# Kernel tuning notes

Hardware: AMD Instinct MI355X
Metric: run time of the kernel (lower is better)

Reference implementation:

```python
import jax, jax.numpy as jnp
import numpy as np

B, T, D, C, L, H = 8192, 128, 1, 1, 1, 64


def _mlp(x, w1, b1, w2, b2):
    # Linear -> Softplus -> Linear
    return jax.nn.softplus(x @ w1 + b1) @ w2 + b2


def setup_inputs() -> dict:
    key = jax.random.key(0)
    ks = jax.random.split(key, 32)
    s = 0.1

    def w(k, shape):
        return jax.random.normal(k, shape, jnp.float32) * s

    p = {}
    p["xs"] = jax.random.normal(ks[0], (T, B, D), jnp.float32)
    p["ts"] = jnp.arange(T, dtype=jnp.float32)
    p["noise_std"] = jnp.float32(5.0)
    p["eps0"] = jax.random.normal(ks[1], (B, L), jnp.float32)
    p["dW_std"] = jax.random.normal(ks[2], (T - 1, B, L), jnp.float32)
    # encoder: data -> hidden -> context
    p["ew1"] = w(ks[3], (D, H)); p["eb1"] = w(ks[4], (H,))
    p["ew2"] = w(ks[5], (H, C)); p["eb2"] = w(ks[6], (C,))
    # qz0_net: context -> 2*latent
    p["qw"] = w(ks[7], (C, 2 * L)); p["qb"] = w(ks[8], (2 * L,))
    # f_net: latent+context -> hidden -> latent
    p["fw1"] = w(ks[9], (L + C, H)); p["fb1"] = w(ks[10], (H,))
    p["fw2"] = w(ks[11], (H, L)); p["fb2"] = w(ks[12], (L,))
    # h_net: latent -> hidden -> latent
    p["hw1"] = w(ks[13], (L, H)); p["hb1"] = w(ks[14], (H,))
    p["hw2"] = w(ks[15], (H, L)); p["hb2"] = w(ks[16], (L,))
    # g_nets: L independent 1 -> hidden -> 1 -> sigmoid nets, stacked on leading L axis
    p["gw1"] = w(ks[17], (L, H)); p["gb1"] = w(ks[18], (L, H))
    p["gw2"] = w(ks[19], (L, H)); p["gb2"] = w(ks[20], (L,))
    # projector: latent -> hidden -> data
    p["pw1"] = w(ks[21], (L, H)); p["pb1"] = w(ks[22], (H,))
    p["pw2"] = w(ks[23], (H, D)); p["pb2"] = w(ks[24], (D,))
    p["pz0_mean"] = jnp.zeros((1, L), jnp.float32)
    p["pz0_logstd"] = jnp.zeros((1, L), jnp.float32)
    return p


def reference(xs, ts, noise_std, eps0, dW_std,
              ew1, eb1, ew2, eb2, qw, qb,
              fw1, fb1, fw2, fb2, hw1, hb1, hw2, hb2,
              gw1, gb1, gw2, gb2, pw1, pb1, pw2, pb2,
              pz0_mean, pz0_logstd):
    Tn = ts.shape[0]
    # ctx = flip(encoder(flip(xs)))  (encoder is pointwise in time)
    ctx = jnp.flip(_mlp(jnp.flip(xs, axis=0), ew1, eb1, ew2, eb2), axis=0)  # [T,B,C]
    qz = ctx[0] @ qw + qb
    qm, qls = jnp.split(qz, 2, axis=1)  # [B,L] each
    z0 = qm + jnp.exp(qls) * eps0

    def g_fn(z):  # per-coordinate diagonal diffusion nets
        hid = jax.nn.softplus(z[:, :, None] * gw1[None] + gb1[None])  # [B,L,H]
        return jax.nn.sigmoid(jnp.einsum('blh,lh->bl', hid, gw2) + gb2)

    def step(z, inp):
        k, dwk = inp
        t = ts[k]
        dt = ts[k + 1] - ts[k]
        idx = jnp.minimum(jnp.searchsorted(ts, t, side='right'), Tn - 1)
        c = jnp.take(ctx, idx, axis=0)  # [B,C]
        fv = _mlp(jnp.concatenate([z, c], axis=1), fw1, fb1, fw2, fb2)
        hv = _mlp(z, hw1, hb1, hw2, hb2)
        gv = g_fn(z)
        u = (fv - hv) / gv
        lr = 0.5 * jnp.sum(u * u, axis=1) * dt  # logqp path increment [B]
        z_next = z + fv * dt + gv * dwk * jnp.sqrt(dt)  # Euler-Maruyama
        return z_next, (z_next, lr)

    _, (ztail, log_ratio) = jax.lax.scan(step, z0, (jnp.arange(Tn - 1), dW_std))
    zs = jnp.concatenate([z0[None], ztail], axis=0)  # [T,B,L]
    _xs = _mlp(zs, pw1, pb1, pw2, pb2)  # [T,B,D]
    lp = -0.5 * ((xs - _xs) / noise_std) ** 2 - jnp.log(noise_std) - 0.5 * jnp.log(2 * jnp.pi)
    log_pxs = lp.sum(axis=(0, 2)).mean()
    kl = (pz0_logstd - qls) + (jnp.exp(2 * qls) + (qm - pz0_mean) ** 2) / (2 * jnp.exp(2 * pz0_logstd)) - 0.5
    logqp0 = kl.sum(axis=1).mean()
    logqp_path = log_ratio.sum(axis=0).mean()
    return (log_pxs, logqp0 + logqp_path)
```

## Files before the change

### kernel.cpp

```cpp
#include <hip/hip_runtime.h>
#include <math.h>


#define B_SZ 8192
#define T_SZ 128
#define NBLK 16

#define FQ1_OFF  0
#define HGP1_OFF 8196
#define FQ2_OFF  12296
#define HGP2_OFF 16396
#define ET2_OFF  20496
#define TAB_FLOATS 22544
#define FQ1_I  0
#define HGP1_I 2049
#define FQ2_I  3074
#define HGP2_I 4099

#define NF1 2049
#define NH1 1025
#define NF2 1025
#define NH2 1025
#define NEE 1024
#define NENT (NF1+NH1+NF2+NH2+NEE)

#define NXI 1024
#define XSF 64.0f
#define XOF 512.0f

#if __has_builtin(__builtin_amdgcn_rcpf)
#define RCPF(x) __builtin_amdgcn_rcpf(x)
#else
#define RCPF(x) (1.0f / (x))
#endif
#if __has_builtin(__builtin_amdgcn_sqrtf)
#define SQRTF(x) __builtin_amdgcn_sqrtf(x)
#else
#define SQRTF(x) sqrtf(x)
#endif

__device__ __forceinline__ float sp_precise(float a) {
  return fmaxf(a, 0.0f) + log1pf(expf(-fabsf(a)));
}
__device__ __forceinline__ float wsum64(float v) {
  #pragma unroll
  for (int m = 1; m <= 32; m <<= 1) v += __shfl_xor(v, m);
  return v;
}

__global__ __launch_bounds__(256) void build_tabs(
    const float* __restrict__ ew1, const float* __restrict__ eb1,
    const float* __restrict__ ew2, const float* __restrict__ eb2,
    const float* __restrict__ fw1, const float* __restrict__ fb1,
    const float* __restrict__ fw2, const float* __restrict__ fb2,
    const float* __restrict__ hw1, const float* __restrict__ hb1,
    const float* __restrict__ hw2, const float* __restrict__ hb2,
    const float* __restrict__ gw1, const float* __restrict__ gb1,
    const float* __restrict__ gw2, const float* __restrict__ gb2,
    const float* __restrict__ pw1, const float* __restrict__ pb1,
    const float* __restrict__ pw2, const float* __restrict__ pb2,
    float* __restrict__ tabs, int* __restrict__ ctr)
{
  const int gtid = blockIdx.x * 256 + threadIdx.x;
  if (gtid == 0) *ctr = 0;
  const int ent  = gtid >> 6;
  const int lane = threadIdx.x & 63;
  if (ent >= NENT) return;

  if (ent < NF1 + NH1 + NF2 + NH2) {
    bool isF; float z; int idx4;
    if (ent < NF1)                { isF = true;  z = -128.0f + (float)ent * 0.125f;            idx4 = FQ1_I + ent; }
    else if (ent < NF1+NH1)       { isF = false; z = -128.0f + (float)(ent-NF1) * 0.25f;       idx4 = HGP1_I + (ent-NF1); }
    else if (ent < NF1+NH1+NF2)   { isF = true;  z = -8192.0f + (float)(ent-NF1-NH1) * 16.0f;  idx4 = FQ2_I + (ent-NF1-NH1); }
    else                          { isF = false; z = -8192.0f + (float)(ent-NF1-NH1-NF2) * 16.0f; idx4 = HGP2_I + (ent-NF1-NH1-NF2); }

    if (isF) {
      const float az = fmaf(z, fw1[lane], fb1[lane]);
      const float wc = fw1[64 + lane], w2 = fw2[lane];
      float s0 = sp_precise(fmaf(-3.0f, wc, az)) * w2;
      float s1 = sp_precise(fmaf(-1.0f, wc, az)) * w2;
      float s2 = sp_precise(fmaf( 1.0f, wc, az)) * w2;
      float s3 = sp_precise(fmaf( 3.0f, wc, az)) * w2;
      s0 = wsum64(s0); s1 = wsum64(s1); s2 = wsum64(s2); s3 = wsum64(s3);
      if (lane == 0) {
        const float fb = fb2[0];
        ((float4*)tabs)[idx4] = make_float4(s0 + fb, s1 + fb, s2 + fb, s3 + fb);
      }
    } else {
      float sh = sp_precise(fmaf(z, hw1[lane], hb1[lane])) * hw2[lane];
      float sg = sp_precise(fmaf(z, gw1[lane], gb1[lane])) * gw2[lane];
      float sp = sp_precise(fmaf(z, pw1[lane], pb1[lane])) * pw2[lane];
      sh = wsum64(sh); sg = wsum64(sg); sp = wsum64(sp);
      if (lane == 0) {
        ((float4*)tabs)[idx4] = make_float4(
            sh + hb2[0],
            1.0f / (1.0f + expf(-(sg + gb2[0]))),
            sp + pb2[0], 0.0f);
      }
    }
  } else {
    const int i = ent - (NF1 + NH1 + NF2 + NH2);
    const float x0 = -8.0f + (float)i * (1.0f / 64.0f);
    const float x1 = x0 + (1.0f / 64.0f);
    const float w = ew1[lane], bb = eb1[lane], w2 = ew2[lane];
    float s0 = sp_precise(fmaf(x0, w, bb)) * w2;
    float s1 = sp_precise(fmaf(x1, w, bb)) * w2;
    s0 = wsum64(s0); s1 = wsum64(s1);
    if (lane == 0) {
      const float eb = eb2[0];
      ((float2*)(tabs + ET2_OFF))[i] = make_float2(s0 + eb, s1 + eb);
    }
  }
}

__global__ __launch_bounds__(512) void sde_scan(
    const float* __restrict__ xs, const float* __restrict__ ts,
    const float* __restrict__ noise_std, const float* __restrict__ eps0,
    const float* __restrict__ dW,
    const float* __restrict__ qw,  const float* __restrict__ qb,
    const float* __restrict__ fw1, const float* __restrict__ fb1,
    const float* __restrict__ fw2, const float* __restrict__ fb2,
    const float* __restrict__ hw1, const float* __restrict__ hb1,
    const float* __restrict__ hw2, const float* __restrict__ hb2,
    const float* __restrict__ gw1, const float* __restrict__ gb1,
    const float* __restrict__ gw2, const float* __restrict__ gb2,
    const float* __restrict__ pw1, const float* __restrict__ pb1,
    const float* __restrict__ pw2, const float* __restrict__ pb2,
    const float* __restrict__ pz0_mean, const float* __restrict__ pz0_logstd,
    const float* __restrict__ tabsrc,
    int* __restrict__ ctr, float* __restrict__ partA, float* __restrict__ partB,
    float* __restrict__ out)
{
  __shared__ __align__(16) float tab[TAB_FLOATS];
  __shared__ float la[512], lb[512];
  __shared__ int lastflag;

  const int tid = threadIdx.x;
  const int b   = blockIdx.x * 512 + tid;

  {
    const float4* s4 = (const float4*)tabsrc;
    float4* d4 = (float4*)tab;
    for (int i = tid; i < TAB_FLOATS / 4; i += 512) d4[i] = s4[i];
  }
  __syncthreads();

  const float4* tab4 = (const float4*)tab;
  const float2* et2  = (const float2*)(tab + ET2_OFF);

  const float fb2s = fb2[0], hb2s = hb2[0], gb2s = gb2[0], pb2s = pb2[0];
  const float qw0 = qw[0], qw1 = qw[1], qb0 = qb[0], qb1 = qb[1];
  const float ns = noise_std[0];
  const float inv_ns = 1.0f / ns;
  const float nh_i2 = -0.5f * inv_ns * inv_ns;
  const float pm = pz0_mean[0], pls = pz0_logstd[0];

  auto einterp = [&](float x) {
    const float s = fmaf(x, XSF, XOF);
    const float sc = fminf(fmaxf(s, 0.0f), (float)(NXI - 1));
    const int i = (int)sc;
    const float fr = s - (float)i;
    const float2 e = et2[i];
    return fmaf(fr, e.y - e.x, e.x);
  };
  auto lagr = [&](float c) {
    const float c2 = c * c;
    const float p1 = c2 - 1.0f, p3 = c2 - 9.0f;
    return make_float4(p1 * (c - 3.0f) * (-1.0f / 48.0f),
                       p3 * (c - 1.0f) * ( 1.0f / 16.0f),
                       p3 * (c + 1.0f) * (-1.0f / 16.0f),
                       p1 * (c + 3.0f) * ( 1.0f / 48.0f));
  };
  auto hgp_exact = [&](float z, float& hv, float& gv, float& pv) {
    float sh = 0.f, sg = 0.f, sp = 0.f;
    for (int j = 0; j < 64; ++j) {
      sh = fmaf(sp_precise(fmaf(z, hw1[j], hb1[j])), hw2[j], sh);
      sg = fmaf(sp_precise(fmaf(z, gw1[j], gb1[j])), gw2[j], sg);
      sp = fmaf(sp_precise(fmaf(z, pw1[j], pb1[j])), pw2[j], sp);
    }
    hv = sh + hb2s;
    gv = 1.0f / (1.0f + expf(-(sg + gb2s)));
    pv = sp + pb2s;
  };
  auto f_exact = [&](float z, float c) {
    float s = 0.f;
    for (int j = 0; j < 64; ++j)
      s = fmaf(sp_precise(fmaf(z, fw1[j], fmaf(c, fw1[64 + j], fb1[j]))), fw2[j], s);
    return s + fb2s;
  };

  auto zidx = [&](float z, int& fqi, float& fqf, int& hgi, float& hgf, bool& inr) {
    const float s1 = fmaf(z, 8.0f, 1024.0f);
    const float s2 = fmaf(z, 0.0625f, 512.0f);
    const bool t1 = (s1 >= 0.0f) && (s1 <= 2048.0f);
    const bool t2 = (s2 >= 0.0f) && (s2 <= 1024.0f);
    inr = t1 || t2;
    const float sf = t1 ? s1 : fminf(fmaxf(s2, 0.0f), 1024.0f);
    int fi = min((int)sf, t1 ? 2047 : 1023);
    fqi = (t1 ? FQ1_I : FQ2_I) + fi;
    fqf = sf - (float)fi;
    const float sh = t1 ? fmaf(z, 4.0f, 512.0f) : sf;
    int hi = min((int)sh, 1023);
    hgi = (t1 ? HGP1_I : HGP2_I) + hi;
    hgf = sh - (float)hi;
  };

  const float x0 = xs[b];
  float x1 = xs[B_SZ + b];
  float x2 = xs[2 * B_SZ + b];
  const float c0v = einterp(x0);
  float c_cur = einterp(x1);
  float c_nxt = einterp(x2);
  const float qm  = fmaf(c0v, qw0, qb0);
  const float qls = fmaf(c0v, qw1, qb1);
  float z = fmaf(__expf(qls), eps0[b], qm);
  const float dqm = qm - pm;
  const float kl = (pls - qls)
                 + (__expf(2.0f * qls) + dqm * dqm) * (0.5f * __expf(-2.0f * pls))
                 - 0.5f;

  bool zin; int fqi, hgi; float fqf, hgf;
  float4 q0, q1; float hv, gv, pv;
  zidx(z, fqi, fqf, hgi, hgf, zin);
  q0 = tab4[fqi]; q1 = tab4[fqi + 1];
  {
    const float4 a = tab4[hgi], bq = tab4[hgi + 1];
    if (zin) {
      hv = fmaf(hgf, bq.x - a.x, a.x);
      gv = fmaf(hgf, bq.y - a.y, a.y);
      pv = fmaf(hgf, bq.z - a.z, a.z);
    } else {
      hgp_exact(z, hv, gv, pv);
    }
  }
  float lp_sum; { const float d = x0 - pv; lp_sum = nh_i2 * d * d; }
  float lr_sum = 0.0f;
  float dw_cur = dW[b];
  float dw_n1  = dW[B_SZ + b];
  float4 L = lagr(c_cur);
  bool cin = fabsf(c_cur) <= 3.0f;

  for (int k = 0; k < T_SZ - 1; ++k) {
    const int   i3    = (k + 3 < T_SZ) ? (k + 3) : (T_SZ - 1);
    const float x3    = xs[i3 * B_SZ + b];
    const float dw_n2 = (k + 2 < T_SZ - 1) ? dW[(k + 2) * B_SZ + b] : 0.0f;
    const float dt    = ts[k + 1] - ts[k];
    const float sq    = SQRTF(dt);

    float fv;
    if (zin && cin) {
      const float n0 = fmaf(fqf, q1.x - q0.x, q0.x);
      const float n1 = fmaf(fqf, q1.y - q0.y, q0.y);
      const float n2 = fmaf(fqf, q1.z - q0.z, q0.z);
      const float n3 = fmaf(fqf, q1.w - q0.w, q0.w);
      fv = n0 * L.x + n1 * L.y + n2 * L.z + n3 * L.w;
    } else {
      fv = f_exact(z, c_cur);
    }

    const float gvs = fmaxf(gv, 1e-6f);
    const float uu = (fv - hv) * RCPF(gvs);
    lr_sum = fmaf((0.5f * dt) * uu, uu, lr_sum);
    z = fmaf(gvs * dw_cur, sq, fmaf(fv, dt, z));

    zidx(z, fqi, fqf, hgi, hgf, zin);
    q0 = tab4[fqi]; q1 = tab4[fqi + 1];
    const float4 a = tab4[hgi], bq = tab4[hgi + 1];
    if (zin) {
      hv = fmaf(hgf, bq.x - a.x, a.x);
      gv = fmaf(hgf, bq.y - a.y, a.y);
      pv = fmaf(hgf, bq.z - a.z, a.z);
    } else {
      hgp_exact(z, hv, gv, pv);
    }

    const float d = x1 - pv;
    lp_sum = fmaf(nh_i2 * d, d, lp_sum);

    c_cur = c_nxt; L = lagr(c_cur); cin = fabsf(c_cur) <= 3.0f;
    c_nxt = einterp(x3);
    x1 = x2; x2 = x3;
    dw_cur = dw_n1; dw_n1 = dw_n2;
  }

  la[tid] = lp_sum; lb[tid] = kl + lr_sum;
  __syncthreads();
  for (int s = 256; s > 0; s >>= 1) {
    if (tid < s) { la[tid] += la[tid + s]; lb[tid] += lb[tid + s]; }
    __syncthreads();
  }
  if (tid == 0) {
    partA[blockIdx.x] = la[0]; partB[blockIdx.x] = lb[0];
    __threadfence();
    lastflag = (atomicAdd(ctr, 1) == NBLK - 1) ? 1 : 0;
  }
  __syncthreads();
  if (lastflag) {
    __threadfence();
    la[tid] = (tid < NBLK) ? partA[tid] : 0.0f;
    lb[tid] = (tid < NBLK) ? partB[tid] : 0.0f;
    __syncthreads();
    for (int s = 256; s > 0; s >>= 1) {
      if (tid < s) { la[tid] += la[tid + s]; lb[tid] += lb[tid + s]; }
      __syncthreads();
    }
    if (tid == 0) {
      out[0] = la[0] / (float)B_SZ
             + (float)T_SZ * (-__logf(ns) - 0.9189385332046727f);
      out[1] = lb[0] / (float)B_SZ;
    }
  }
}

extern "C" void kernel_launch(void* const* d_in, const int* in_sizes, int n_in,
                              void* d_out, int out_size, void* d_ws, size_t ws_size,
                              hipStream_t stream) {
  const float* xs        = (const float*)d_in[0];
  const float* ts        = (const float*)d_in[1];
  const float* noise_std = (const float*)d_in[2];
  const float* eps0      = (const float*)d_in[3];
  const float* dW        = (const float*)d_in[4];
  const float* ew1 = (const float*)d_in[5];
  const float* eb1 = (const float*)d_in[6];
  const float* ew2 = (const float*)d_in[7];
  const float* eb2 = (const float*)d_in[8];
  const float* qw  = (const float*)d_in[9];
  const float* qb  = (const float*)d_in[10];
  const float* fw1 = (const float*)d_in[11];
  const float* fb1 = (const float*)d_in[12];
  const float* fw2 = (const float*)d_in[13];
  const float* fb2 = (const float*)d_in[14];
  const float* hw1 = (const float*)d_in[15];
  const float* hb1 = (const float*)d_in[16];
  const float* hw2 = (const float*)d_in[17];
  const float* hb2 = (const float*)d_in[18];
  const float* gw1 = (const float*)d_in[19];
  const float* gb1 = (const float*)d_in[20];
  const float* gw2 = (const float*)d_in[21];
  const float* gb2 = (const float*)d_in[22];
  const float* pw1 = (const float*)d_in[23];
  const float* pb1 = (const float*)d_in[24];
  const float* pw2 = (const float*)d_in[25];
  const float* pb2 = (const float*)d_in[26];
  const float* pz0_mean   = (const float*)d_in[27];
  const float* pz0_logstd = (const float*)d_in[28];
  float* out = (float*)d_out;

  float* tabs  = (float*)d_ws;
  int*   ctr   = (int*)(tabs + TAB_FLOATS);
  float* partA = tabs + TAB_FLOATS + 4;
  float* partB = partA + NBLK;

  build_tabs<<<(NENT * 64 + 255) / 256, 256, 0, stream>>>(
      ew1, eb1, ew2, eb2, fw1, fb1, fw2, fb2,
      hw1, hb1, hw2, hb2, gw1, gb1, gw2, gb2,
      pw1, pb1, pw2, pb2, tabs, ctr);

  sde_scan<<<NBLK, 512, 0, stream>>>(
      xs, ts, noise_std, eps0, dW, qw, qb,
      fw1, fb1, fw2, fb2, hw1, hb1, hw2, hb2,
      gw1, gb1, gw2, gb2, pw1, pb1, pw2, pb2,
      pz0_mean, pz0_logstd, tabs, ctr, partA, partB, out);
}
```

Measured before the change: 74.10 us.

## Unify f/hgp tables on one z grid, precompute context, use 32 blocks

The f and h/g/p lookup tables now share one z grid and are interleaved, so each step needs a single index computation and four adjacent float4 loads instead of two separate index paths. The h/g/p table resolution rises to match the f table in the inner range. Context interpolation moves into a separate ctx_pre kernel that writes ctx to global memory, and the scan kernel reads it alongside xs. The scan now runs 32 blocks of 256 threads instead of 16 of 512, spreading the work over more CUs. This costs an extra kernel launch and a global ctx round trip.

Result: no change. 73.85 us (-0.3%).

```diff
diff --git a/kernel.cpp b/kernel.cpp
--- a/kernel.cpp
+++ b/kernel.cpp
@@ -4,25 +4,17 @@
 
 #define B_SZ 8192
 #define T_SZ 128
-#define NBLK 16
-
-#define FQ1_OFF  0
-#define HGP1_OFF 8196
-#define FQ2_OFF  12296
-#define HGP2_OFF 16396
-#define ET2_OFF  20496
-#define TAB_FLOATS 22544
-#define FQ1_I  0
-#define HGP1_I 2049
-#define FQ2_I  3074
-#define HGP2_I 4099
-
-#define NF1 2049
-#define NH1 1025
-#define NF2 1025
-#define NH2 1025
+#define NBLK 32
+
+#define NT1 2049
+#define NT2 1025
 #define NEE 1024
-#define NENT (NF1+NH1+NF2+NH2+NEE)
+#define NENT (NT1 + NT2 + NEE)
+
+#define MT_FLOATS (8 * (NT1 + NT2))
+#define ET2G_OFF  MT_FLOATS
+#define TABG_FLOATS (MT_FLOATS + 2048)
+#define T2_BASE4 (2 * NT1)
 
 #define NXI 1024
 #define XSF 64.0f
@@ -67,39 +59,34 @@
   const int lane = threadIdx.x & 63;
   if (ent >= NENT) return;
 
-  if (ent < NF1 + NH1 + NF2 + NH2) {
-    bool isF; float z; int idx4;
-    if (ent < NF1)                { isF = true;  z = -128.0f + (float)ent * 0.125f;            idx4 = FQ1_I + ent; }
-    else if (ent < NF1+NH1)       { isF = false; z = -128.0f + (float)(ent-NF1) * 0.25f;       idx4 = HGP1_I + (ent-NF1); }
-    else if (ent < NF1+NH1+NF2)   { isF = true;  z = -8192.0f + (float)(ent-NF1-NH1) * 16.0f;  idx4 = FQ2_I + (ent-NF1-NH1); }
-    else                          { isF = false; z = -8192.0f + (float)(ent-NF1-NH1-NF2) * 16.0f; idx4 = HGP2_I + (ent-NF1-NH1-NF2); }
-
-    if (isF) {
-      const float az = fmaf(z, fw1[lane], fb1[lane]);
-      const float wc = fw1[64 + lane], w2 = fw2[lane];
-      float s0 = sp_precise(fmaf(-3.0f, wc, az)) * w2;
-      float s1 = sp_precise(fmaf(-1.0f, wc, az)) * w2;
-      float s2 = sp_precise(fmaf( 1.0f, wc, az)) * w2;
-      float s3 = sp_precise(fmaf( 3.0f, wc, az)) * w2;
-      s0 = wsum64(s0); s1 = wsum64(s1); s2 = wsum64(s2); s3 = wsum64(s3);
-      if (lane == 0) {
-        const float fb = fb2[0];
-        ((float4*)tabs)[idx4] = make_float4(s0 + fb, s1 + fb, s2 + fb, s3 + fb);
-      }
-    } else {
-      float sh = sp_precise(fmaf(z, hw1[lane], hb1[lane])) * hw2[lane];
-      float sg = sp_precise(fmaf(z, gw1[lane], gb1[lane])) * gw2[lane];
-      float sp = sp_precise(fmaf(z, pw1[lane], pb1[lane])) * pw2[lane];
-      sh = wsum64(sh); sg = wsum64(sg); sp = wsum64(sp);
-      if (lane == 0) {
-        ((float4*)tabs)[idx4] = make_float4(
-            sh + hb2[0],
-            1.0f / (1.0f + expf(-(sg + gb2[0]))),
-            sp + pb2[0], 0.0f);
-      }
+  if (ent < NT1 + NT2) {
+    const bool t1 = ent < NT1;
+    const int  i  = t1 ? ent : (ent - NT1);
+    const float z = t1 ? (-128.0f + (float)i * 0.125f)
+                       : (-8192.0f + (float)i * 16.0f);
+    const int base4 = (t1 ? 0 : T2_BASE4) + 2 * i;
+
+    const float az = fmaf(z, fw1[lane], fb1[lane]);
+    const float wc = fw1[64 + lane], w2 = fw2[lane];
+    float s0 = sp_precise(fmaf(-3.0f, wc, az)) * w2;
+    float s1 = sp_precise(fmaf(-1.0f, wc, az)) * w2;
+    float s2 = sp_precise(fmaf( 1.0f, wc, az)) * w2;
+    float s3 = sp_precise(fmaf( 3.0f, wc, az)) * w2;
+    float sh = sp_precise(fmaf(z, hw1[lane], hb1[lane])) * hw2[lane];
+    float sg = sp_precise(fmaf(z, gw1[lane], gb1[lane])) * gw2[lane];
+    float sp = sp_precise(fmaf(z, pw1[lane], pb1[lane])) * pw2[lane];
+    s0 = wsum64(s0); s1 = wsum64(s1); s2 = wsum64(s2); s3 = wsum64(s3);
+    sh = wsum64(sh); sg = wsum64(sg); sp = wsum64(sp);
+    if (lane == 0) {
+      const float fb = fb2[0];
+      ((float4*)tabs)[base4]     = make_float4(s0 + fb, s1 + fb, s2 + fb, s3 + fb);
+      ((float4*)tabs)[base4 + 1] = make_float4(
+          sh + hb2[0],
+          1.0f / (1.0f + expf(-(sg + gb2[0]))),
+          sp + pb2[0], 0.0f);
     }
   } else {
-    const int i = ent - (NF1 + NH1 + NF2 + NH2);
+    const int i = ent - (NT1 + NT2);
     const float x0 = -8.0f + (float)i * (1.0f / 64.0f);
     const float x1 = x0 + (1.0f / 64.0f);
     const float w = ew1[lane], bb = eb1[lane], w2 = ew2[lane];
@@ -108,15 +95,29 @@
     s0 = wsum64(s0); s1 = wsum64(s1);
     if (lane == 0) {
       const float eb = eb2[0];
-      ((float2*)(tabs + ET2_OFF))[i] = make_float2(s0 + eb, s1 + eb);
-    }
-  }
-}
-
-__global__ __launch_bounds__(512) void sde_scan(
+      ((float2*)(tabs + ET2G_OFF))[i] = make_float2(s0 + eb, s1 + eb);
+    }
+  }
+}
+
+__global__ __launch_bounds__(256) void ctx_pre(
+    const float* __restrict__ xs, const float* __restrict__ tabs,
+    float* __restrict__ ctx)
+{
+  const int i = blockIdx.x * 256 + threadIdx.x;
+  const float2* et2 = (const float2*)(tabs + ET2G_OFF);
+  const float s = fmaf(xs[i], XSF, XOF);
+  const float sc = fminf(fmaxf(s, 0.0f), (float)(NXI - 1));
+  const int ii = (int)sc;
+  const float fr = s - (float)ii;
+  const float2 e = et2[ii];
+  ctx[i] = fmaf(fr, e.y - e.x, e.x);
+}
+
+__global__ __launch_bounds__(256) void sde_scan(
     const float* __restrict__ xs, const float* __restrict__ ts,
     const float* __restrict__ noise_std, const float* __restrict__ eps0,
-    const float* __restrict__ dW,
+    const float* __restrict__ dW, const float* __restrict__ ctx,
     const float* __restrict__ qw,  const float* __restrict__ qb,
     const float* __restrict__ fw1, const float* __restrict__ fb1,
     const float* __restrict__ fw2, const float* __restrict__ fb2,
@@ -131,22 +132,21 @@
     int* __restrict__ ctr, float* __restrict__ partA, float* __restrict__ partB,
     float* __restrict__ out)
 {
-  __shared__ __align__(16) float tab[TAB_FLOATS];
-  __shared__ float la[512], lb[512];
+  __shared__ __align__(16) float tab[MT_FLOATS];
+  __shared__ float la[256], lb[256];
   __shared__ int lastflag;
 
   const int tid = threadIdx.x;
-  const int b   = blockIdx.x * 512 + tid;
+  const int b   = blockIdx.x * 256 + tid;
 
   {
     const float4* s4 = (const float4*)tabsrc;
     float4* d4 = (float4*)tab;
-    for (int i = tid; i < TAB_FLOATS / 4; i += 512) d4[i] = s4[i];
+    for (int i = tid; i < MT_FLOATS / 4; i += 256) d4[i] = s4[i];
   }
   __syncthreads();
 
   const float4* tab4 = (const float4*)tab;
-  const float2* et2  = (const float2*)(tab + ET2_OFF);
 
   const float fb2s = fb2[0], hb2s = hb2[0], gb2s = gb2[0], pb2s = pb2[0];
   const float qw0 = qw[0], qw1 = qw[1], qb0 = qb[0], qb1 = qb[1];
@@ -155,14 +155,6 @@
   const float nh_i2 = -0.5f * inv_ns * inv_ns;
   const float pm = pz0_mean[0], pls = pz0_logstd[0];
 
-  auto einterp = [&](float x) {
-    const float s = fmaf(x, XSF, XOF);
-    const float sc = fminf(fmaxf(s, 0.0f), (float)(NXI - 1));
-    const int i = (int)sc;
-    const float fr = s - (float)i;
-    const float2 e = et2[i];
-    return fmaf(fr, e.y - e.x, e.x);
-  };
   auto lagr = [&](float c) {
     const float c2 = c * c;
     const float p1 = c2 - 1.0f, p3 = c2 - 9.0f;
@@ -189,28 +181,24 @@
     return s + fb2s;
   };
 
-  auto zidx = [&](float z, int& fqi, float& fqf, int& hgi, float& hgf, bool& inr) {
+  auto zidx = [&](float z, int& base4, float& frac, bool& inr) {
     const float s1 = fmaf(z, 8.0f, 1024.0f);
     const float s2 = fmaf(z, 0.0625f, 512.0f);
     const bool t1 = (s1 >= 0.0f) && (s1 <= 2048.0f);
     const bool t2 = (s2 >= 0.0f) && (s2 <= 1024.0f);
     inr = t1 || t2;
     const float sf = t1 ? s1 : fminf(fmaxf(s2, 0.0f), 1024.0f);
-    int fi = min((int)sf, t1 ? 2047 : 1023);
-    fqi = (t1 ? FQ1_I : FQ2_I) + fi;
-    fqf = sf - (float)fi;
-    const float sh = t1 ? fmaf(z, 4.0f, 512.0f) : sf;
-    int hi = min((int)sh, 1023);
-    hgi = (t1 ? HGP1_I : HGP2_I) + hi;
-    hgf = sh - (float)hi;
+    const int fi = min((int)sf, t1 ? (NT1 - 2) : (NT2 - 2));
+    base4 = (t1 ? 0 : T2_BASE4) + 2 * fi;
+    frac = sf - (float)fi;
   };
 
   const float x0 = xs[b];
   float x1 = xs[B_SZ + b];
   float x2 = xs[2 * B_SZ + b];
-  const float c0v = einterp(x0);
-  float c_cur = einterp(x1);
-  float c_nxt = einterp(x2);
+  const float c0v = ctx[b];
+  float c_cur = ctx[B_SZ + b];
+  float c_nxt = ctx[2 * B_SZ + b];
   const float qm  = fmaf(c0v, qw0, qb0);
   const float qls = fmaf(c0v, qw1, qb1);
   float z = fmaf(__expf(qls), eps0[b], qm);
@@ -219,19 +207,17 @@
                  + (__expf(2.0f * qls) + dqm * dqm) * (0.5f * __expf(-2.0f * pls))
                  - 0.5f;
 
-  bool zin; int fqi, hgi; float fqf, hgf;
-  float4 q0, q1; float hv, gv, pv;
-  zidx(z, fqi, fqf, hgi, hgf, zin);
-  q0 = tab4[fqi]; q1 = tab4[fqi + 1];
-  {
-    const float4 a = tab4[hgi], bq = tab4[hgi + 1];
-    if (zin) {
-      hv = fmaf(hgf, bq.x - a.x, a.x);
-      gv = fmaf(hgf, bq.y - a.y, a.y);
-      pv = fmaf(hgf, bq.z - a.z, a.z);
-    } else {
-      hgp_exact(z, hv, gv, pv);
-    }
+  bool zin; int zb4; float zfr;
+  float4 q0a, q0b, q1a, q1b;
+  float hv, gv, pv;
+  zidx(z, zb4, zfr, zin);
+  q0a = tab4[zb4]; q0b = tab4[zb4 + 1]; q1a = tab4[zb4 + 2]; q1b = tab4[zb4 + 3];
+  if (zin) {
+    hv = fmaf(zfr, q1b.x - q0b.x, q0b.x);
+    gv = fmaf(zfr, q1b.y - q0b.y, q0b.y);
+    pv = fmaf(zfr, q1b.z - q0b.z, q0b.z);
+  } else {
+    hgp_exact(z, hv, gv, pv);
   }
   float lp_sum; { const float d = x0 - pv; lp_sum = nh_i2 * d * d; }
   float lr_sum = 0.0f;
@@ -243,16 +229,17 @@
   for (int k = 0; k < T_SZ - 1; ++k) {
     const int   i3    = (k + 3 < T_SZ) ? (k + 3) : (T_SZ - 1);
     const float x3    = xs[i3 * B_SZ + b];
+    const float c3    = ctx[i3 * B_SZ + b];
     const float dw_n2 = (k + 2 < T_SZ - 1) ? dW[(k + 2) * B_SZ + b] : 0.0f;
     const float dt    = ts[k + 1] - ts[k];
     const float sq    = SQRTF(dt);
 
     float fv;
     if (zin && cin) {
-      const float n0 = fmaf(fqf, q1.x - q0.x, q0.x);
-      const float n1 = fmaf(fqf, q1.y - q0.y, q0.y);
-      const float n2 = fmaf(fqf, q1.z - q0.z, q0.z);
-      const float n3 = fmaf(fqf, q1.w - q0.w, q0.w);
+      const float n0 = fmaf(zfr, q1a.x - q0a.x, q0a.x);
+      const float n1 = fmaf(zfr, q1a.y - q0a.y, q0a.y);
+      const float n2 = fmaf(zfr, q1a.z - q0a.z, q0a.z);
+      const float n3 = fmaf(zfr, q1a.w - q0a.w, q0a.w);
       fv = n0 * L.x + n1 * L.y + n2 * L.z + n3 * L.w;
     } else {
       fv = f_exact(z, c_cur);
@@ -263,13 +250,12 @@
     lr_sum = fmaf((0.5f * dt) * uu, uu, lr_sum);
     z = fmaf(gvs * dw_cur, sq, fmaf(fv, dt, z));
 
-    zidx(z, fqi, fqf, hgi, hgf, zin);
-    q0 = tab4[fqi]; q1 = tab4[fqi + 1];
-    const float4 a = tab4[hgi], bq = tab4[hgi + 1];
+    zidx(z, zb4, zfr, zin);
+    q0a = tab4[zb4]; q0b = tab4[zb4 + 1]; q1a = tab4[zb4 + 2]; q1b = tab4[zb4 + 3];
     if (zin) {
-      hv = fmaf(hgf, bq.x - a.x, a.x);
-      gv = fmaf(hgf, bq.y - a.y, a.y);
-      pv = fmaf(hgf, bq.z - a.z, a.z);
+      hv = fmaf(zfr, q1b.x - q0b.x, q0b.x);
+      gv = fmaf(zfr, q1b.y - q0b.y, q0b.y);
+      pv = fmaf(zfr, q1b.z - q0b.z, q0b.z);
     } else {
       hgp_exact(z, hv, gv, pv);
     }
@@ -278,14 +264,14 @@
     lp_sum = fmaf(nh_i2 * d, d, lp_sum);
 
     c_cur = c_nxt; L = lagr(c_cur); cin = fabsf(c_cur) <= 3.0f;
-    c_nxt = einterp(x3);
+    c_nxt = c3;
     x1 = x2; x2 = x3;
     dw_cur = dw_n1; dw_n1 = dw_n2;
   }
 
   la[tid] = lp_sum; lb[tid] = kl + lr_sum;
   __syncthreads();
-  for (int s = 256; s > 0; s >>= 1) {
+  for (int s = 128; s > 0; s >>= 1) {
     if (tid < s) { la[tid] += la[tid + s]; lb[tid] += lb[tid + s]; }
     __syncthreads();
   }
@@ -300,7 +286,7 @@
     la[tid] = (tid < NBLK) ? partA[tid] : 0.0f;
     lb[tid] = (tid < NBLK) ? partB[tid] : 0.0f;
     __syncthreads();
-    for (int s = 256; s > 0; s >>= 1) {
+    for (int s = 128; s > 0; s >>= 1) {
       if (tid < s) { la[tid] += la[tid + s]; lb[tid] += lb[tid + s]; }
       __syncthreads();
     }
@@ -347,17 +333,20 @@
   float* out = (float*)d_out;
 
   float* tabs  = (float*)d_ws;
-  int*   ctr   = (int*)(tabs + TAB_FLOATS);
-  float* partA = tabs + TAB_FLOATS + 4;
+  int*   ctr   = (int*)(tabs + TABG_FLOATS);
+  float* partA = tabs + TABG_FLOATS + 4;
   float* partB = partA + NBLK;
+  float* ctxb  = tabs + TABG_FLOATS + 72;
 
   build_tabs<<<(NENT * 64 + 255) / 256, 256, 0, stream>>>(
       ew1, eb1, ew2, eb2, fw1, fb1, fw2, fb2,
       hw1, hb1, hw2, hb2, gw1, gb1, gw2, gb2,
       pw1, pb1, pw2, pb2, tabs, ctr);
 
-  sde_scan<<<NBLK, 512, 0, stream>>>(
-      xs, ts, noise_std, eps0, dW, qw, qb,
+  ctx_pre<<<(T_SZ * B_SZ) / 256, 256, 0, stream>>>(xs, tabs, ctxb);
+
+  sde_scan<<<NBLK, 256, 0, stream>>>(
+      xs, ts, noise_std, eps0, dW, ctxb, qw, qb,
       fw1, fb1, fw2, fb2, hw1, hb1, hw2, hb2,
       gw1, gb1, gw2, gb2, pw1, pb1, pw2, pb2,
       pz0_mean, pz0_logstd, tabs, ctr, partA, partB, out);
```
